# Optimization experiments

Hardware: AMD Instinct MI355X
Metric: run time of the kernel (lower is better)

Reference implementation:

```python
import jax, jax.numpy as jnp
import numpy as np
import math

NUM_HEADS = 8
DIM = 512
HEAD_DIM = DIM // NUM_HEADS
SCALE = HEAD_DIM ** -0.5
RP = 2            # remove_pad = kernel_size//2 * 2 for kernel_size=3
EPS_GN = 1e-5     # GroupNorm eps
EPS_L1 = 1e-12    # F.normalize eps


def _conv(x, w, b):
    # x: [B, Cin, H, W], w: [Cout, Cin, 3, 3] (OIHW), VALID padding, stride 1
    y = jax.lax.conv_general_dilated(x, w, (1, 1), 'VALID',
                                     dimension_numbers=('NCHW', 'OIHW', 'NCHW'))
    return y + b[None, :, None, None]


def _gn_per_channel(x, g, b):
    # GroupNorm with num_groups == num_channels: per-channel norm over (H, W)
    mu = x.mean(axis=(-2, -1), keepdims=True)
    var = x.var(axis=(-2, -1), keepdims=True)
    xn = (x - mu) * jax.lax.rsqrt(var + EPS_GN)
    return xn * g[None, :, None, None] + b[None, :, None, None]


def _ppe(rpe, c1w, c1b, g1w, g1b, c2w, c2b, g2w, g2b):
    # PeripheralPositionEncoding: rpe [side^2, side^2, 4*H] -> [1, H, N, N], N=(side-2*RP)^2
    nr, _, d = rpe.shape
    side = int(round(math.sqrt(nr)))
    s2 = side - 2 * RP
    x = rpe.reshape(side, side, side, side, d)          # i j k l d
    x = x[RP:side - RP, RP:side - RP]                   # trim i, j borders
    x = x.transpose(0, 1, 4, 2, 3).reshape(s2 * s2, d, side, side)  # (ij) d k l
    x = jax.nn.relu(_gn_per_channel(_conv(x, c1w, c1b), g1w, g1b))
    x = _gn_per_channel(_conv(x, c2w, c2b), g2w, g2b)   # [(ij), H, s2, s2]
    y = x.reshape(s2 * s2, NUM_HEADS, s2 * s2).transpose(1, 0, 2)[None]  # [1,H,N,N]
    return jax.nn.sigmoid(y)


def setup_inputs() -> dict:
    key = jax.random.key(0)
    ks = jax.random.split(key, 12)
    B, N = 8, 1024            # N = (36 - 4)^2
    side = 36
    cin = NUM_HEADS * 4       # 32
    inp = {
        'x': jax.random.normal(ks[0], (B, N, DIM), jnp.float32),
        'rpe_embed': jax.random.normal(ks[1], (side * side, side * side, cin), jnp.float32),
        'wqkv': jax.random.normal(ks[2], (3 * DIM, DIM), jnp.float32) * 0.02,
        'wproj': jax.random.normal(ks[3], (DIM, DIM), jnp.float32) * 0.02,
        'bproj': jnp.zeros((DIM,), jnp.float32),
        'c1w': jax.random.normal(ks[4], (cin, cin, 3, 3), jnp.float32) * 0.02,
        'c1b': jnp.zeros((cin,), jnp.float32),
        'g1w': jnp.ones((cin,), jnp.float32),
        'g1b': jnp.zeros((cin,), jnp.float32),
        'c2w': jax.random.normal(ks[5], (NUM_HEADS, cin, 3, 3), jnp.float32) * 0.02,
        'c2b': jnp.zeros((NUM_HEADS,), jnp.float32),
        'g2w': jnp.ones((NUM_HEADS,), jnp.float32),        # norm_init[1] = 1.0
        'g2b': jnp.zeros((NUM_HEADS,), jnp.float32),       # norm_init[0] = 0.0
    }
    return inp


def reference(x, rpe_embed, wqkv, wproj, bproj, c1w, c1b, g1w, g1b, c2w, c2b, g2w, g2b):
    B, N, D = x.shape
    H, HD = NUM_HEADS, HEAD_DIM
    qkv = x @ wqkv.T                                   # [B, N, 3D]
    q, k, v = jnp.split(qkv, 3, axis=-1)
    def heads(t):
        return t.reshape(B, N, H, HD).transpose(0, 2, 1, 3)  # [B, H, N, HD]
    q, k, v = heads(q), heads(k), heads(v)
    dots = jnp.einsum('bhnd,bhmd->bhnm', q, k) * SCALE
    dots = jnp.exp(dots - dots.max(axis=-1, keepdims=True))  # stable exp-score
    w = _ppe(rpe_embed, c1w, c1b, g1w, g1b, c2w, c2b, g2w, g2b)  # [1,H,N,N]
    attn = w * dots
    attn = attn / jnp.maximum(jnp.abs(attn).sum(axis=-1, keepdims=True), EPS_L1)  # L1 normalize
    out = jnp.einsum('bhnm,bhmd->bhnd', attn, v)
    out = out.transpose(0, 2, 1, 3).reshape(B, N, D)
    return out @ wproj.T + bproj
```

## Files before the change

kernel.cpp:

```cpp
#include <hip/hip_runtime.h>
#include <hip/hip_fp16.h>


typedef __attribute__((ext_vector_type(8))) short bf16x8;
typedef __attribute__((ext_vector_type(8))) _Float16 f16x8;
typedef __attribute__((ext_vector_type(4))) float f32x4;

__device__ __forceinline__ unsigned short f2bf(float f) {
  unsigned u = __builtin_bit_cast(unsigned, f);
  u += 0x7FFFu + ((u >> 16) & 1u);
  return (unsigned short)(u >> 16);
}

__global__ __launch_bounds__(256) void wprep(
    const float* __restrict__ c1w, const float* __restrict__ c2w,
    unsigned short* __restrict__ w1frag, unsigned short* __restrict__ w2frag)
{
  int t = blockIdx.x * 256 + threadIdx.x;
  if (t < 9216) {
    int j = t & 7, ln = (t >> 3) & 63, ctap = t >> 9;
    int tap = ctap >> 1, ct = ctap & 1;
    int oc = 2 * (ln & 15) + ct, ic = (ln >> 4) * 8 + j;
    w1frag[t] = __half_as_ushort(__float2half(c1w[(oc * 32 + ic) * 9 + tap]));
  }
  if (t < 4608) {
    int j = t & 7, ln = (t >> 3) & 63, tap = t >> 9;
    int oc = (ln & 15) & 7, ic = (ln >> 4) * 8 + j;
    w2frag[t] = __half_as_ushort(__float2half(c2w[(oc * 32 + ic) * 9 + tap]));
  }
}

template<bool OUT_BF16>
__global__ __launch_bounds__(256) void gemm_f16_bt(
    const float* __restrict__ A, const float* __restrict__ B,
    void* __restrict__ Cv, const float* __restrict__ bias,
    int M, int N, int K)
{
  __shared__ __align__(16) _Float16 As[128 * 40];
  __shared__ __align__(16) _Float16 Bs[128 * 40];
  const int tid = threadIdx.x;
  const int wv = tid >> 6, ln = tid & 63, lr = ln & 15, lq = ln >> 4;
  const int wm = wv >> 1, wn = wv & 1;
  const int m0 = blockIdx.y * 128, n0 = blockIdx.x * 128;

  f32x4 acc[4][4];
#pragma unroll
  for (int i = 0; i < 4; i++)
#pragma unroll
    for (int j = 0; j < 4; j++) acc[i][j] = (f32x4){0.f, 0.f, 0.f, 0.f};

  const int sr = tid >> 1, sk = (tid & 1) * 16;
  const float* Ap = A + (size_t)(m0 + sr) * K + sk;
  const float* Bp = B + (size_t)(n0 + sr) * K + sk;

  for (int k0 = 0; k0 < K; k0 += 32) {
    float4 av0 = *(const float4*)(Ap + k0);
    float4 av1 = *(const float4*)(Ap + k0 + 4);
    float4 av2 = *(const float4*)(Ap + k0 + 8);
    float4 av3 = *(const float4*)(Ap + k0 + 12);
    float4 bv0 = *(const float4*)(Bp + k0);
    float4 bv1 = *(const float4*)(Bp + k0 + 4);
    float4 bv2 = *(const float4*)(Bp + k0 + 8);
    float4 bv3 = *(const float4*)(Bp + k0 + 12);
    __syncthreads();
    {
      f16x8 p0, p1, r0, r1;
      p0[0]=(_Float16)av0.x; p0[1]=(_Float16)av0.y; p0[2]=(_Float16)av0.z; p0[3]=(_Float16)av0.w;
      p0[4]=(_Float16)av1.x; p0[5]=(_Float16)av1.y; p0[6]=(_Float16)av1.z; p0[7]=(_Float16)av1.w;
      p1[0]=(_Float16)av2.x; p1[1]=(_Float16)av2.y; p1[2]=(_Float16)av2.z; p1[3]=(_Float16)av2.w;
      p1[4]=(_Float16)av3.x; p1[5]=(_Float16)av3.y; p1[6]=(_Float16)av3.z; p1[7]=(_Float16)av3.w;
      r0[0]=(_Float16)bv0.x; r0[1]=(_Float16)bv0.y; r0[2]=(_Float16)bv0.z; r0[3]=(_Float16)bv0.w;
      r0[4]=(_Float16)bv1.x; r0[5]=(_Float16)bv1.y; r0[6]=(_Float16)bv1.z; r0[7]=(_Float16)bv1.w;
      r1[0]=(_Float16)bv2.x; r1[1]=(_Float16)bv2.y; r1[2]=(_Float16)bv2.z; r1[3]=(_Float16)bv2.w;
      r1[4]=(_Float16)bv3.x; r1[5]=(_Float16)bv3.y; r1[6]=(_Float16)bv3.z; r1[7]=(_Float16)bv3.w;
      *(f16x8*)&As[sr * 40 + sk] = p0;
      *(f16x8*)&As[sr * 40 + sk + 8] = p1;
      *(f16x8*)&Bs[sr * 40 + sk] = r0;
      *(f16x8*)&Bs[sr * 40 + sk + 8] = r1;
    }
    __syncthreads();
    f16x8 af[4], bf[4];
#pragma unroll
    for (int mf = 0; mf < 4; mf++)
      af[mf] = *(const f16x8*)&As[(wm * 64 + mf * 16 + lr) * 40 + lq * 8];
#pragma unroll
    for (int nf = 0; nf < 4; nf++)
      bf[nf] = *(const f16x8*)&Bs[(wn * 64 + nf * 16 + lr) * 40 + lq * 8];
#pragma unroll
    for (int mf = 0; mf < 4; mf++)
#pragma unroll
      for (int nf = 0; nf < 4; nf++)
        acc[mf][nf] = __builtin_amdgcn_mfma_f32_16x16x32_f16(af[mf], bf[nf], acc[mf][nf], 0, 0, 0);
  }

#pragma unroll
  for (int mf = 0; mf < 4; mf++)
#pragma unroll
    for (int reg = 0; reg < 4; reg++) {
      const int row = m0 + wm * 64 + mf * 16 + lq * 4 + reg;
#pragma unroll
      for (int nf = 0; nf < 4; nf++) {
        const int col = n0 + wn * 64 + nf * 16 + lr;
        float v = acc[mf][nf][reg];
        if (bias) v += bias[col];
        if (OUT_BF16) ((unsigned short*)Cv)[(size_t)row * N + col] = f2bf(v);
        else          ((float*)Cv)[(size_t)row * N + col] = v;
      }
    }
}

__global__ __launch_bounds__(1024, 1) void conv_fused3(
    const float* __restrict__ rpe,
    const unsigned short* __restrict__ w1frag, const unsigned short* __restrict__ w2frag,
    const float* __restrict__ g1, const float* __restrict__ b1,
    const float* __restrict__ g2, const float* __restrict__ b2,
    float* __restrict__ wout)
{
  extern __shared__ __align__(16) char smem[];
  unsigned short* inA = (unsigned short*)smem;
  unsigned short* yB  = (unsigned short*)(smem + 82944);
  float* statA = (float*)(smem + 156928);
  float* aL    = (float*)(smem + 157184);
  float* cL    = aL + 32;
  float* transF = (float*)smem;

  const int tid = threadIdx.x;
  const int wv = tid >> 6, ln = tid & 63;
  const int lr = ln & 15, lq = ln >> 4;
  const int p = blockIdx.x;

  if (tid < 64) statA[tid] = 0.f;

  const float* src = rpe + (size_t)(((p >> 5) + 2) * 36 + (p & 31) + 2) * 41472;
  for (int t = tid; t < 10368; t += 1024) {
    int pix = t >> 3, dq = (t & 7) << 2;
    float4 v = *(const float4*)(src + pix * 32 + dq);
    __half2 h0 = __floats2half2_rn(v.x, v.y);
    __half2 h1 = __floats2half2_rn(v.z, v.w);
    uint2 u; u.x = __builtin_bit_cast(unsigned, h0); u.y = __builtin_bit_cast(unsigned, h1);
    *(uint2*)&inA[(dq >> 3) * 10368 + pix * 8 + (dq & 7)] = u;
  }

  f16x8 w1f[2][9];
#pragma unroll
  for (int ct = 0; ct < 2; ct++)
#pragma unroll
    for (int tap = 0; tap < 9; tap++)
      w1f[ct][tap] = *(const f16x8*)&w1frag[((tap * 2 + ct) * 64 + ln) * 8];
  __syncthreads();

  constexpr int OFF1[9] = {0, 8, 16, 288, 296, 304, 576, 584, 592};
  const unsigned short* inAg = inA + lq * 10368;
  float s0 = 0.f, q0 = 0.f, s1 = 0.f, q1 = 0.f;
  for (int t0 = wv; t0 < 64; t0 += 32) {
    const int tA = t0, tB = t0 + 16;
    const int mA = tA * 16 + lr, mB = tB * 16 + lr;
    const unsigned short* abA = inAg + ((mA / 34) * 36 + (mA % 34)) * 8;
    const unsigned short* abB = inAg + ((mB / 34) * 36 + (mB % 34)) * 8;
    f32x4 cA0 = {0.f,0.f,0.f,0.f}, cA1 = {0.f,0.f,0.f,0.f};
    f32x4 cB0 = {0.f,0.f,0.f,0.f}, cB1 = {0.f,0.f,0.f,0.f};
#pragma unroll
    for (int tap = 0; tap < 9; tap++) {
      f16x8 avA = *(const f16x8*)(abA + OFF1[tap]);
      f16x8 avB = *(const f16x8*)(abB + OFF1[tap]);
      cA0 = __builtin_amdgcn_mfma_f32_16x16x32_f16(avA, w1f[0][tap], cA0, 0, 0, 0);
      cA1 = __builtin_amdgcn_mfma_f32_16x16x32_f16(avA, w1f[1][tap], cA1, 0, 0, 0);
      cB0 = __builtin_amdgcn_mfma_f32_16x16x32_f16(avB, w1f[0][tap], cB0, 0, 0, 0);
      cB1 = __builtin_amdgcn_mfma_f32_16x16x32_f16(avB, w1f[1][tap], cB1, 0, 0, 0);
    }
#pragma unroll
    for (int r = 0; r < 4; r++) {
      int moA = tA * 16 + lq * 4 + r;
      float v0 = cA0[r], v1 = cA1[r];
      unsigned u = (unsigned)__half_as_ushort(__float2half(v0))
                 | ((unsigned)__half_as_ushort(__float2half(v1)) << 16);
      *(unsigned*)&yB[(lr >> 2) * 9248 + moA * 8 + ((lr * 2) & 7)] = u;
      s0 += v0; q0 += v0 * v0; s1 += v1; q1 += v1 * v1;
      int moB = tB * 16 + lq * 4 + r;
      float w0 = cB0[r], w1 = cB1[r];
      unsigned u2 = (unsigned)__half_as_ushort(__float2half(w0))
                  | ((unsigned)__half_as_ushort(__float2half(w1)) << 16);
      *(unsigned*)&yB[(lr >> 2) * 9248 + moB * 8 + ((lr * 2) & 7)] = u2;
      s0 += w0; q0 += w0 * w0; s1 += w1; q1 += w1 * w1;
    }
  }
  if (wv < 9) {
    int t = wv + 64;
    int m = t * 16 + lr;
    int ms = m < 1155 ? m : 1155;
    const unsigned short* ab = inAg + ((ms / 34) * 36 + (ms % 34)) * 8;
    f32x4 c0 = {0.f,0.f,0.f,0.f}, c1v = {0.f,0.f,0.f,0.f};
#pragma unroll
    for (int tap = 0; tap < 9; tap++) {
      f16x8 av = *(const f16x8*)(ab + OFF1[tap]);
      c0  = __builtin_amdgcn_mfma_f32_16x16x32_f16(av, w1f[0][tap], c0, 0, 0, 0);
      c1v = __builtin_amdgcn_mfma_f32_16x16x32_f16(av, w1f[1][tap], c1v, 0, 0, 0);
    }
#pragma unroll
    for (int r = 0; r < 4; r++) {
      int mo = t * 16 + lq * 4 + r;
      if (mo < 1156) {
        float v0 = c0[r], v1 = c1v[r];
        unsigned u = (unsigned)__half_as_ushort(__float2half(v0))
                   | ((unsigned)__half_as_ushort(__float2half(v1)) << 16);
        *(unsigned*)&yB[(lr >> 2) * 9248 + mo * 8 + ((lr * 2) & 7)] = u;
        s0 += v0; q0 += v0 * v0; s1 += v1; q1 += v1 * v1;
      }
    }
  }
#pragma unroll
  for (int off = 16; off < 64; off <<= 1) {
    s0 += __shfl_xor(s0, off); q0 += __shfl_xor(q0, off);
    s1 += __shfl_xor(s1, off); q1 += __shfl_xor(q1, off);
  }
  if (ln < 16) {
    atomicAdd(&statA[ln], s0);      atomicAdd(&statA[16 + ln], q0);
    atomicAdd(&statA[32 + ln], s1); atomicAdd(&statA[48 + ln], q1);
  }
  __syncthreads();
  if (tid < 32) {
    int cti = tid >> 4, lri = tid & 15;
    float s = statA[cti * 32 + lri];
    float q = statA[cti * 32 + 16 + lri];
    int ch = 2 * lri + cti;
    float mu = s * (1.f / 1156.f);
    float var = q * (1.f / 1156.f) - mu * mu;
    float a_ = rsqrtf(var + 1e-5f) * g1[ch];
    aL[ch] = a_; cL[ch] = b1[ch] - mu * a_;
  }
  if (tid < 16) statA[tid] = 0.f;
  __syncthreads();

  {
    int g = tid >> 8, ocb = g * 8;
    unsigned short* yg = yB + g * 9248;
    for (int pix = (tid & 255); pix < 1156; pix += 256) {
      f16x8 raw = *(const f16x8*)&yg[pix * 8];
      f16x8 outv;
#pragma unroll
      for (int e = 0; e < 8; e++) {
        float v = (float)raw[e];
        outv[e] = (_Float16)fmaxf(v * aL[ocb + e] + cL[ocb + e], 0.f);
      }
      *(f16x8*)&yg[pix * 8] = outv;
    }
  }
  __syncthreads();

  f16x8 w2f[9];
#pragma unroll
  for (int tap = 0; tap < 9; tap++)
    w2f[tap] = *(const f16x8*)&w2frag[(tap * 64 + ln) * 8];

  constexpr int OFF2[9] = {0, 8, 16, 272, 280, 288, 544, 552, 560};
  const unsigned short* yBg = yB + lq * 9248;
  float s2 = 0.f, q2 = 0.f;
#pragma unroll
  for (int t0 = 0; t0 < 2; t0++) {
    const int tA = wv + t0 * 32, tB = tA + 16;
    const int mA = tA * 16 + lr, mB = tB * 16 + lr;
    const unsigned short* abA = yBg + ((mA >> 5) * 34 + (mA & 31)) * 8;
    const unsigned short* abB = yBg + ((mB >> 5) * 34 + (mB & 31)) * 8;
    f32x4 ccA = {0.f,0.f,0.f,0.f}, ccB = {0.f,0.f,0.f,0.f};
#pragma unroll
    for (int tap = 0; tap < 9; tap++) {
      f16x8 avA = *(const f16x8*)(abA + OFF2[tap]);
      f16x8 avB = *(const f16x8*)(abB + OFF2[tap]);
      ccA = __builtin_amdgcn_mfma_f32_16x16x32_f16(avA, w2f[tap], ccA, 0, 0, 0);
      ccB = __builtin_amdgcn_mfma_f32_16x16x32_f16(avB, w2f[tap], ccB, 0, 0, 0);
    }
#pragma unroll
    for (int r = 0; r < 4; r++) {
      float vA = ccA[r], vB = ccB[r];
      s2 += vA + vB; q2 += vA * vA + vB * vB;
      if (lr < 8) {
        transF[lr * 1032 + tA * 16 + lq * 4 + r] = vA;
        transF[lr * 1032 + tB * 16 + lq * 4 + r] = vB;
      }
    }
  }
#pragma unroll
  for (int off = 16; off < 64; off <<= 1) {
    s2 += __shfl_xor(s2, off); q2 += __shfl_xor(q2, off);
  }
  if (ln < 8) { atomicAdd(&statA[ln], s2); atomicAdd(&statA[8 + ln], q2); }
  __syncthreads();
  if (tid < 8) {
    float s = statA[tid], q = statA[8 + tid];
    float mu = s * (1.f / 1024.f);
    float var = q * (1.f / 1024.f) - mu * mu;
    float a_ = rsqrtf(var + 1e-5f) * g2[tid];
    aL[tid] = a_; cL[tid] = b2[tid] - mu * a_;
  }
  __syncthreads();

  for (int idx = tid; idx < 2048; idx += 1024) {
    int oc = idx >> 8, p4 = (idx & 255) << 2;
    float4 v = *(const float4*)&transF[oc * 1032 + p4];
    float a_ = aL[oc], c_ = cL[oc];
    float4 o;
    o.x = 1.f / (1.f + __expf(-(v.x * a_ + c_)));
    o.y = 1.f / (1.f + __expf(-(v.y * a_ + c_)));
    o.z = 1.f / (1.f + __expf(-(v.z * a_ + c_)));
    o.w = 1.f / (1.f + __expf(-(v.w * a_ + c_)));
    *(float4*)(wout + ((size_t)oc << 20) + ((size_t)p << 10) + p4) = o;
  }
}

__global__ __launch_bounds__(256) void attn_kernel(
    const unsigned short* __restrict__ qkv,
    const float* __restrict__ wppe,
    float* __restrict__ oh)
{
  __shared__ __align__(16) unsigned short k_lds[64 * 72];
  __shared__ __align__(16) unsigned short v_lds[64 * 72];
  __shared__ __align__(16) unsigned short p_lds[4 * 16 * 72];
  const int tid = threadIdx.x;
  const int wv = tid >> 6, ln = tid & 63;
  const int lr = ln & 15, lq = ln >> 4;
  const int b = blockIdx.y >> 3, h = blockIdx.y & 7;
  const int n0 = blockIdx.x << 6;

  const size_t qoff = (size_t)((b << 10) + n0 + (wv << 4) + lr) * 1536 + (h << 6);
  bf16x8 qf0 = *(const bf16x8*)(qkv + qoff + lq * 8);
  bf16x8 qf1 = *(const bf16x8*)(qkv + qoff + 32 + lq * 8);

  f32x4 acc[4];
#pragma unroll
  for (int dt = 0; dt < 4; dt++) acc[dt] = (f32x4){0.f, 0.f, 0.f, 0.f};
  float den[4] = {0.f, 0.f, 0.f, 0.f};
  const float* wp = wppe + ((size_t)h << 20);

  for (int m0 = 0; m0 < 1024; m0 += 64) {
    __syncthreads();
    for (int t = tid; t < 512; t += 256) {
      int m = t >> 3, dq = t & 7;
      const unsigned short* kr = qkv + (size_t)((b << 10) + m0 + m) * 1536 + 512 + (h << 6) + dq * 8;
      *(uint4*)&k_lds[m * 72 + dq * 8] = *(const uint4*)kr;
      uint4 vvv = *(const uint4*)(kr + 512);
      unsigned short tmp[8];
      *(uint4*)tmp = vvv;
#pragma unroll
      for (int i = 0; i < 8; i++) {
        int d = dq * 8 + i;
        v_lds[d * 72 + (m ^ (((d >> 3) & 7) << 3))] = tmp[i];
      }
    }
    __syncthreads();

    f32x4 s[4];
#pragma unroll
    for (int mt = 0; mt < 4; mt++) {
      const unsigned short* kb = &k_lds[(mt * 16 + lr) * 72 + lq * 8];
      f32x4 cz = (f32x4){0.f, 0.f, 0.f, 0.f};
      cz = __builtin_amdgcn_mfma_f32_16x16x32_bf16(qf0, *(const bf16x8*)kb, cz, 0, 0, 0);
      cz = __builtin_amdgcn_mfma_f32_16x16x32_bf16(qf1, *(const bf16x8*)(kb + 32), cz, 0, 0, 0);
      s[mt] = cz;
    }
#pragma unroll
    for (int mt = 0; mt < 4; mt++)
#pragma unroll
      for (int reg = 0; reg < 4; reg++) {
        int rrow = lq * 4 + reg;
        float wvl = wp[(size_t)(n0 + (wv << 4) + rrow) * 1024 + (m0 + mt * 16 + lr)];
        float pv = wvl * __expf(s[mt][reg] * 0.125f);
        den[reg] += pv;
        p_lds[((wv << 4) + rrow) * 72 + mt * 16 + lr] = f2bf(pv);
      }
    const unsigned short* pb = &p_lds[((wv << 4) + lr) * 72];
    bf16x8 pa0 = *(const bf16x8*)(pb + lq * 8);
    bf16x8 pa1 = *(const bf16x8*)(pb + 32 + lq * 8);
#pragma unroll
    for (int dt = 0; dt < 4; dt++) {
      int d = dt * 16 + lr;
      int sw = ((d >> 3) & 7) << 3;
      const unsigned short* vb = &v_lds[d * 72];
      acc[dt] = __builtin_amdgcn_mfma_f32_16x16x32_bf16(pa0, *(const bf16x8*)(vb + ((lq * 8) ^ sw)), acc[dt], 0, 0, 0);
      acc[dt] = __builtin_amdgcn_mfma_f32_16x16x32_bf16(pa1, *(const bf16x8*)(vb + ((32 + lq * 8) ^ sw)), acc[dt], 0, 0, 0);
    }
  }
#pragma unroll
  for (int off = 1; off < 16; off <<= 1)
#pragma unroll
    for (int reg = 0; reg < 4; reg++) den[reg] += __shfl_xor(den[reg], off);
#pragma unroll
  for (int dt = 0; dt < 4; dt++)
#pragma unroll
    for (int reg = 0; reg < 4; reg++) {
      size_t row = (size_t)((b << 10) + n0 + (wv << 4) + lq * 4 + reg);
      oh[row * 512 + (h << 6) + dt * 16 + lr] = acc[dt][reg] / den[reg];
    }
}

extern "C" void kernel_launch(void* const* d_in, const int* in_sizes, int n_in,
                              void* d_out, int out_size, void* d_ws, size_t ws_size,
                              hipStream_t stream) {
  (void)in_sizes; (void)n_in; (void)out_size; (void)ws_size;
  const float* x     = (const float*)d_in[0];
  const float* rpe   = (const float*)d_in[1];
  const float* wqkv  = (const float*)d_in[2];
  const float* wproj = (const float*)d_in[3];
  const float* bproj = (const float*)d_in[4];
  const float* c1w   = (const float*)d_in[5];
  const float* g1w   = (const float*)d_in[7];
  const float* g1b   = (const float*)d_in[8];
  const float* c2w   = (const float*)d_in[9];
  const float* g2w   = (const float*)d_in[11];
  const float* g2b   = (const float*)d_in[12];
  float* out = (float*)d_out;

  char* ws = (char*)d_ws;
  unsigned short* qkv_bf = (unsigned short*)ws;
  float* wppe = (float*)(ws + 25165824);
  float* ohb  = (float*)(ws + 58720256);
  unsigned short* w1frag = (unsigned short*)(ws + 75497472);
  unsigned short* w2frag = (unsigned short*)(ws + 75515904);

  wprep<<<36, 256, 0, stream>>>(c1w, c2w, w1frag, w2frag);

  gemm_f16_bt<true><<<dim3(12, 64), 256, 0, stream>>>(x, wqkv, qkv_bf, nullptr, 8192, 1536, 512);

  const int ldsC = 157440;
  hipFuncSetAttribute(reinterpret_cast<const void*>(&conv_fused3),
                      hipFuncAttributeMaxDynamicSharedMemorySize, ldsC);
  conv_fused3<<<1024, 1024, ldsC, stream>>>(rpe, w1frag, w2frag, g1w, g1b, g2w, g2b, wppe);

  attn_kernel<<<dim3(16, 64), 256, 0, stream>>>(qkv_bf, wppe, ohb);

  gemm_f16_bt<false><<<dim3(4, 64), 256, 0, stream>>>(ohb, wproj, out, bproj, 8192, 512, 512);
}
```

Baseline: 205.7 us.

## Pre-convert GEMM weights to fp16, stage PPE weights in LDS, emit fp16 attention output

A new kernel converts wqkv and wproj to fp16 once per call, so both GEMMs load half-width B tiles with no per-tile conversion. The attention kernel writes its output in fp16, which halves that intermediate buffer, and the projection GEMM reads it directly as fp16. The attention kernel also stages each 64x64 tile of PPE weights into LDS with coalesced float4 loads, replacing scattered per-element global reads. The costs are an extra launch and a small added rounding step on the attention output, which is already rounded to fp16 inside the GEMM anyway.

```diff
diff --git a/kernel.cpp b/kernel.cpp
--- a/kernel.cpp
+++ b/kernel.cpp
@@ -30,9 +30,30 @@
   }
 }
 
-template<bool OUT_BF16>
+__global__ __launch_bounds__(256) void wcvt(
+    const float* __restrict__ wqkv, const float* __restrict__ wproj,
+    __half* __restrict__ wqkvh, __half* __restrict__ wprojh)
+{
+  int t = blockIdx.x * 256 + threadIdx.x;
+  if (t < 196608) {
+    float4 v = ((const float4*)wqkv)[t];
+    __half2 h0 = __floats2half2_rn(v.x, v.y);
+    __half2 h1 = __floats2half2_rn(v.z, v.w);
+    uint2 u; u.x = __builtin_bit_cast(unsigned, h0); u.y = __builtin_bit_cast(unsigned, h1);
+    *(uint2*)&wqkvh[t * 4] = u;
+  } else {
+    int t2 = t - 196608;
+    float4 v = ((const float4*)wproj)[t2];
+    __half2 h0 = __floats2half2_rn(v.x, v.y);
+    __half2 h1 = __floats2half2_rn(v.z, v.w);
+    uint2 u; u.x = __builtin_bit_cast(unsigned, h0); u.y = __builtin_bit_cast(unsigned, h1);
+    *(uint2*)&wprojh[t2 * 4] = u;
+  }
+}
+
+template<bool A_HALF, bool OUT_BF16>
 __global__ __launch_bounds__(256) void gemm_f16_bt(
-    const float* __restrict__ A, const float* __restrict__ B,
+    const void* __restrict__ Av, const __half* __restrict__ Bh,
     void* __restrict__ Cv, const float* __restrict__ bias,
     int M, int N, int K)
 {
@@ -50,34 +71,37 @@
     for (int j = 0; j < 4; j++) acc[i][j] = (f32x4){0.f, 0.f, 0.f, 0.f};
 
   const int sr = tid >> 1, sk = (tid & 1) * 16;
-  const float* Ap = A + (size_t)(m0 + sr) * K + sk;
-  const float* Bp = B + (size_t)(n0 + sr) * K + sk;
+  const float*  Af = (const float*)Av;
+  const __half* Ah = (const __half*)Av;
 
   for (int k0 = 0; k0 < K; k0 += 32) {
-    float4 av0 = *(const float4*)(Ap + k0);
-    float4 av1 = *(const float4*)(Ap + k0 + 4);
-    float4 av2 = *(const float4*)(Ap + k0 + 8);
-    float4 av3 = *(const float4*)(Ap + k0 + 12);
-    float4 bv0 = *(const float4*)(Bp + k0);
-    float4 bv1 = *(const float4*)(Bp + k0 + 4);
-    float4 bv2 = *(const float4*)(Bp + k0 + 8);
-    float4 bv3 = *(const float4*)(Bp + k0 + 12);
+    uint4 ha0, ha1;
+    float4 av0, av1, av2, av3;
+    if (A_HALF) {
+      ha0 = *(const uint4*)(Ah + (size_t)(m0 + sr) * K + k0 + sk);
+      ha1 = *(const uint4*)(Ah + (size_t)(m0 + sr) * K + k0 + sk + 8);
+    } else {
+      const float* Ap = Af + (size_t)(m0 + sr) * K + k0 + sk;
+      av0 = *(const float4*)(Ap);      av1 = *(const float4*)(Ap + 4);
+      av2 = *(const float4*)(Ap + 8);  av3 = *(const float4*)(Ap + 12);
+    }
+    uint4 hb0 = *(const uint4*)(Bh + (size_t)(n0 + sr) * K + k0 + sk);
+    uint4 hb1 = *(const uint4*)(Bh + (size_t)(n0 + sr) * K + k0 + sk + 8);
     __syncthreads();
-    {
-      f16x8 p0, p1, r0, r1;
+    if (A_HALF) {
+      *(uint4*)&As[sr * 40 + sk] = ha0;
+      *(uint4*)&As[sr * 40 + sk + 8] = ha1;
+    } else {
+      f16x8 p0, p1;
       p0[0]=(_Float16)av0.x; p0[1]=(_Float16)av0.y; p0[2]=(_Float16)av0.z; p0[3]=(_Float16)av0.w;
       p0[4]=(_Float16)av1.x; p0[5]=(_Float16)av1.y; p0[6]=(_Float16)av1.z; p0[7]=(_Float16)av1.w;
       p1[0]=(_Float16)av2.x; p1[1]=(_Float16)av2.y; p1[2]=(_Float16)av2.z; p1[3]=(_Float16)av2.w;
       p1[4]=(_Float16)av3.x; p1[5]=(_Float16)av3.y; p1[6]=(_Float16)av3.z; p1[7]=(_Float16)av3.w;
-      r0[0]=(_Float16)bv0.x; r0[1]=(_Float16)bv0.y; r0[2]=(_Float16)bv0.z; r0[3]=(_Float16)bv0.w;
-      r0[4]=(_Float16)bv1.x; r0[5]=(_Float16)bv1.y; r0[6]=(_Float16)bv1.z; r0[7]=(_Float16)bv1.w;
-      r1[0]=(_Float16)bv2.x; r1[1]=(_Float16)bv2.y; r1[2]=(_Float16)bv2.z; r1[3]=(_Float16)bv2.w;
-      r1[4]=(_Float16)bv3.x; r1[5]=(_Float16)bv3.y; r1[6]=(_Float16)bv3.z; r1[7]=(_Float16)bv3.w;
       *(f16x8*)&As[sr * 40 + sk] = p0;
       *(f16x8*)&As[sr * 40 + sk + 8] = p1;
-      *(f16x8*)&Bs[sr * 40 + sk] = r0;
-      *(f16x8*)&Bs[sr * 40 + sk + 8] = r1;
-    }
+    }
+    *(uint4*)&Bs[sr * 40 + sk] = hb0;
+    *(uint4*)&Bs[sr * 40 + sk + 8] = hb1;
     __syncthreads();
     f16x8 af[4], bf[4];
 #pragma unroll
@@ -310,11 +334,12 @@
 __global__ __launch_bounds__(256) void attn_kernel(
     const unsigned short* __restrict__ qkv,
     const float* __restrict__ wppe,
-    float* __restrict__ oh)
+    __half* __restrict__ oh)
 {
   __shared__ __align__(16) unsigned short k_lds[64 * 72];
   __shared__ __align__(16) unsigned short v_lds[64 * 72];
   __shared__ __align__(16) unsigned short p_lds[4 * 16 * 72];
+  __shared__ __align__(16) float w_lds[64 * 68];
   const int tid = threadIdx.x;
   const int wv = tid >> 6, ln = tid & 63;
   const int lr = ln & 15, lq = ln >> 4;
@@ -346,6 +371,11 @@
         v_lds[d * 72 + (m ^ (((d >> 3) & 7) << 3))] = tmp[i];
       }
     }
+    for (int t = tid; t < 1024; t += 256) {
+      int r = t >> 4, c4 = (t & 15) << 2;
+      float4 v = *(const float4*)(wp + (size_t)(n0 + r) * 1024 + m0 + c4);
+      *(float4*)&w_lds[r * 68 + c4] = v;
+    }
     __syncthreads();
 
     f32x4 s[4];
@@ -362,7 +392,7 @@
 #pragma unroll
       for (int reg = 0; reg < 4; reg++) {
         int rrow = lq * 4 + reg;
-        float wvl = wp[(size_t)(n0 + (wv << 4) + rrow) * 1024 + (m0 + mt * 16 + lr)];
+        float wvl = w_lds[((wv << 4) + rrow) * 68 + (mt << 4) + lr];
         float pv = wvl * __expf(s[mt][reg] * 0.125f);
         den[reg] += pv;
         p_lds[((wv << 4) + rrow) * 72 + mt * 16 + lr] = f2bf(pv);
@@ -388,7 +418,7 @@
 #pragma unroll
     for (int reg = 0; reg < 4; reg++) {
       size_t row = (size_t)((b << 10) + n0 + (wv << 4) + lq * 4 + reg);
-      oh[row * 512 + (h << 6) + dt * 16 + lr] = acc[dt][reg] / den[reg];
+      oh[row * 512 + (h << 6) + dt * 16 + lr] = __float2half(acc[dt][reg] / den[reg]);
     }
 }
 
@@ -412,20 +442,25 @@
   char* ws = (char*)d_ws;
   unsigned short* qkv_bf = (unsigned short*)ws;
   float* wppe = (float*)(ws + 25165824);
-  float* ohb  = (float*)(ws + 58720256);
-  unsigned short* w1frag = (unsigned short*)(ws + 75497472);
-  unsigned short* w2frag = (unsigned short*)(ws + 75515904);
+  __half* oh_h = (__half*)(ws + 58720256);
+  unsigned short* w1frag = (unsigned short*)(ws + 67108864);
+  unsigned short* w2frag = (unsigned short*)(ws + 67127296);
+  __half* wqkvh = (__half*)(ws + 67136512);
+  __half* wprojh = (__half*)(ws + 68709376);
 
   wprep<<<36, 256, 0, stream>>>(c1w, c2w, w1frag, w2frag);
-
-  gemm_f16_bt<true><<<dim3(12, 64), 256, 0, stream>>>(x, wqkv, qkv_bf, nullptr, 8192, 1536, 512);
+  wcvt<<<1024, 256, 0, stream>>>(wqkv, wproj, wqkvh, wprojh);
+
+  gemm_f16_bt<false, true><<<dim3(12, 64), 256, 0, stream>>>(
+      x, wqkvh, qkv_bf, nullptr, 8192, 1536, 512);
 
   const int ldsC = 157440;
   hipFuncSetAttribute(reinterpret_cast<const void*>(&conv_fused3),
                       hipFuncAttributeMaxDynamicSharedMemorySize, ldsC);
   conv_fused3<<<1024, 1024, ldsC, stream>>>(rpe, w1frag, w2frag, g1w, g1b, g2w, g2b, wppe);
 
-  attn_kernel<<<dim3(16, 64), 256, 0, stream>>>(qkv_bf, wppe, ohb);
-
-  gemm_f16_bt<false><<<dim3(4, 64), 256, 0, stream>>>(ohb, wproj, out, bproj, 8192, 512, 512);
-}
+  attn_kernel<<<dim3(16, 64), 256, 0, stream>>>(qkv_bf, wppe, oh_h);
+
+  gemm_f16_bt<true, false><<<dim3(4, 64), 256, 0, stream>>>(
+      oh_h, wprojh, out, bproj, 8192, 512, 512);
+}
```

Result: slower. 248.2 us (+20.7%).
